# Kernel tuning notes

Measured on AMD Instinct MI355X. Metric: run time of the kernel, lower is better.

The kernel has to match this reference:

```python
import jax, jax.numpy as jnp
import numpy as np

N_NODES = 100000
N_EDGES = 1600000
N_FEATS = 128
N_CLASSES = 40
K_HOPS = 3


def setup_inputs() -> dict:
    key = jax.random.key(0)
    k1, k2, k3, k4 = jax.random.split(key, 4)
    x = jax.random.normal(k1, (N_NODES, N_FEATS), dtype=jnp.float32)
    edge_index = jax.random.randint(k2, (2, N_EDGES), 0, N_NODES, dtype=jnp.int64)
    edge_weight = jax.random.uniform(k3, (N_EDGES,), dtype=jnp.float32)
    # Linear layer of SGConv (bias=False): [num_feats, num_classes]
    W = jax.random.normal(k4, (N_FEATS, N_CLASSES), dtype=jnp.float32) / np.sqrt(N_FEATS)
    return {"x": x, "edge_index": edge_index, "edge_weight": edge_weight, "W": W}


def reference(x, edge_index, edge_weight, W):
    # SGConv forward: gcn_norm (symmetric, no self-loops), K hops of
    # edge-weighted gather/scatter aggregation, then linear (lin_first=False).
    row, col = edge_index[0], edge_index[1]
    # symmetric normalization: deg from target-node scatter of edge weights
    deg = jax.ops.segment_sum(edge_weight, col, num_segments=N_NODES)
    deg_inv_sqrt = jnp.where(deg > 0, jax.lax.rsqrt(jnp.maximum(deg, 1e-30)), 0.0)
    norm = deg_inv_sqrt[row] * edge_weight * deg_inv_sqrt[col]  # [E]
    h = x
    for _ in range(K_HOPS):
        msgs = h[row] * norm[:, None]                 # [E, F] gather + scale
        h = jax.ops.segment_sum(msgs, col, num_segments=N_NODES)  # [N, F] scatter-add
    return h @ W  # [N, num_classes]
```

## Files before the change

kernel.cpp:

```cpp
#include <hip/hip_runtime.h>
#include <hip/hip_fp16.h>

namespace {
constexpr int NN = 100000;
constexpr int NE = 1600000;
constexpr int NF = 128;
constexpr int NC = 40;
constexpr int HP = 64;
constexpr int NB = (NN + 255) / 256;
constexpr int EPB = 4096;
constexpr int EBK = (NE + EPB - 1) / EPB;
constexpr int CAP = 6144;
constexpr float FIX = 1048576.0f;
constexpr int NPB = 51;
constexpr int HB  = (NN + NPB - 1) / NPB;
constexpr int TS  = 2048;
}

struct alignas(16) H8 { __half2 a, b, c, d; };

__device__ inline __half2 f2h2(float x, float y) {
    return __halves2half2(__float2half_rn(x), __float2half_rn(y));
}

__global__ __launch_bounds__(256) void k_fused(const int* __restrict__ col,
                                               const int* __restrict__ row,
                                               const float* __restrict__ w,
                                               unsigned int* __restrict__ cursor,
                                               int2* __restrict__ bstage,
                                               const float* __restrict__ x,
                                               const float* __restrict__ W,
                                               __half* __restrict__ g0) {
    __shared__ char sb[20480];
    int t = threadIdx.x;
    if (blockIdx.x < (unsigned)EBK) {
        unsigned int* lhist = (unsigned int*)sb;
        unsigned int* lbase = lhist + NB;
        unsigned int* lrank = lbase + NB;
        for (int i = t; i < NB; i += 256) { lhist[i] = 0u; lrank[i] = 0u; }
        __syncthreads();
        int e0 = blockIdx.x * EPB;
        int e1 = min(e0 + EPB, NE);
        for (int e = e0 + t; e < e1; e += 256)
            atomicAdd(&lhist[col[e] >> 8], 1u);
        __syncthreads();
        for (int i = t; i < NB; i += 256) {
            unsigned c = lhist[i];
            lbase[i] = c ? atomicAdd(&cursor[i], c) : 0u;
        }
        __syncthreads();
        for (int e = e0 + t; e < e1; e += 256) {
            int c = col[e];
            int b = c >> 8;
            unsigned r = atomicAdd(&lrank[b], 1u);
            int2 v;
            v.x = (row[e] & 0x1FFFF) | ((c & 255) << 17);
            v.y = __float_as_int(w[e]);
            bstage[(size_t)b * CAP + lbase[b] + r] = v;
        }
    } else {
        float4* lW = (float4*)sb;
        {
            const float4* Wg = (const float4*)W;
#pragma unroll
            for (int i = 0; i < 5; ++i) lW[t + i * 256] = Wg[t + i * 256];
        }
        __syncthreads();
        int n = (blockIdx.x - EBK) * 256 + t;
        if (n >= NN) return;
        const float4* xr = (const float4*)(x + (size_t)n * NF);
        float acc[NC];
#pragma unroll
        for (int j = 0; j < NC; ++j) acc[j] = 0.f;
        for (int k4 = 0; k4 < NF / 4; ++k4) {
            float4 xv = xr[k4];
#pragma unroll
            for (int kk = 0; kk < 4; ++kk) {
                float xk = (kk == 0) ? xv.x : (kk == 1) ? xv.y : (kk == 2) ? xv.z : xv.w;
                int k = k4 * 4 + kk;
#pragma unroll
                for (int j4 = 0; j4 < 10; ++j4) {
                    float4 wv = lW[k * 10 + j4];
                    acc[j4 * 4 + 0] += xk * wv.x;
                    acc[j4 * 4 + 1] += xk * wv.y;
                    acc[j4 * 4 + 2] += xk * wv.z;
                    acc[j4 * 4 + 3] += xk * wv.w;
                }
            }
        }
        H8* o = (H8*)(g0 + (size_t)n * HP);
#pragma unroll
        for (int g = 0; g < 5; ++g) {
            H8 v;
            v.a = f2h2(acc[g * 8 + 0], acc[g * 8 + 1]);
            v.b = f2h2(acc[g * 8 + 2], acc[g * 8 + 3]);
            v.c = f2h2(acc[g * 8 + 4], acc[g * 8 + 5]);
            v.d = f2h2(acc[g * 8 + 6], acc[g * 8 + 7]);
            o[g] = v;
        }
    }
}

__global__ __launch_bounds__(512) void k_bscan(const unsigned int* __restrict__ cursor,
                                               int* __restrict__ bbase,
                                               int* __restrict__ offs) {
    __shared__ int s[512];
    int t = threadIdx.x;
    int v = (t < NB) ? (int)cursor[t] : 0;
    s[t] = v;
    __syncthreads();
    for (int off = 1; off < 512; off <<= 1) {
        int add = (t >= off) ? s[t - off] : 0;
        __syncthreads();
        s[t] += add;
        __syncthreads();
    }
    if (t < NB) bbase[t] = s[t] - v;
    if (t == NB) bbase[NB] = s[NB - 1];
    if (t == 0)  offs[NN] = NE;
}

__global__ __launch_bounds__(256) void k_sort(const int2* __restrict__ bstage,
                                              const int* __restrict__ bbase,
                                              int* __restrict__ offs,
                                              float* __restrict__ invdis,
                                              int2* __restrict__ pair,
                                              __half* __restrict__ g0) {
    __shared__ unsigned long long lpk[256];
    __shared__ int ls[256];
    __shared__ float ldis[256];
    __shared__ unsigned int lrank[256];
    int t = threadIdx.x;
    int b = blockIdx.x;
    int base = bbase[b];
    int cnt  = bbase[b + 1] - base;
    lpk[t] = 0ull;
    lrank[t] = 0u;
    __syncthreads();
    const int2* bs = bstage + (size_t)b * CAP;
    for (int j = t; j < cnt; j += 256) {
        int2 s = bs[j];
        int cl = (s.x >> 17) & 255;
        unsigned long long q =
            (unsigned long long)(unsigned)(__int_as_float(s.y) * FIX + 0.5f);
        atomicAdd(&lpk[cl], (1ull << 40) | q);
    }
    __syncthreads();
    int myc = (int)(lpk[t] >> 40);
    float deg = (float)(lpk[t] & ((1ull << 40) - 1)) * (1.0f / FIX);
    float dis = (deg > 0.f) ? rsqrtf(deg) : 0.f;
    ldis[t] = dis;
    ls[t] = myc;
    __syncthreads();
    for (int off = 1; off < 256; off <<= 1) {
        int add = (t >= off) ? ls[t - off] : 0;
        __syncthreads();
        ls[t] += add;
        __syncthreads();
    }
    int start = ls[t] - myc;
    int n = b * 256 + t;
    if (n < NN) {
        offs[n] = base + start;
        invdis[n] = sqrtf(fmaxf(deg, 0.f));
        *(float*)(g0 + (size_t)n * HP + 40) = dis;
    }
    ls[t] = start;
    __syncthreads();
    for (int j = t; j < cnt; j += 256) {
        int2 s = bs[j];
        int cl = (s.x >> 17) & 255;
        unsigned r = atomicAdd(&lrank[cl], 1u);
        float d = ldis[cl];
        int2 v;
        v.x = s.x & 0x1FFFF;
        v.y = __float_as_int(__int_as_float(s.y) * d * d);
        pair[base + ls[cl] + r] = v;
    }
}

template <bool FINAL, bool WD>
__global__ __launch_bounds__(256) void k_hop(const int* __restrict__ offs,
                                             const int2* __restrict__ pair,
                                             const __half* __restrict__ hin,
                                             __half* __restrict__ houth,
                                             float* __restrict__ houtf,
                                             const float* __restrict__ invdis) {
    __shared__ int2 tile[TS];
    __shared__ int erange[2];
    int t = threadIdx.x;
    int g = t / 5;
    int n = blockIdx.x * NPB + g;
    bool active = (t < NPB * 5) && (n < NN);
    int vo = (t - g * 5) * 8;
    int s0 = 0, s1 = 0;
    if (active) {
        s0 = offs[n];
        s1 = offs[n + 1];
    }
    if (t == 0) {
        int n0 = blockIdx.x * NPB;
        int nl = min(n0 + NPB, NN);
        erange[0] = offs[n0];
        erange[1] = offs[nl];
    }
    __syncthreads();
    int E0 = erange[0], E1 = erange[1];
    float acc[8];
#pragma unroll
    for (int j = 0; j < 8; ++j) acc[j] = 0.f;
    int i = s0;
#define ACC8(m, wgt) { float2 f_;                                        \
    f_ = __half22float2((m).a); acc[0] += f_.x * (wgt); acc[1] += f_.y * (wgt); \
    f_ = __half22float2((m).b); acc[2] += f_.x * (wgt); acc[3] += f_.y * (wgt); \
    f_ = __half22float2((m).c); acc[4] += f_.x * (wgt); acc[5] += f_.y * (wgt); \
    f_ = __half22float2((m).d); acc[6] += f_.x * (wgt); acc[7] += f_.y * (wgt); }
    for (int t0 = E0; t0 < E1; t0 += TS) {
        int lim = min(t0 + TS, E1);
        int cnt = lim - t0;
        for (int j = t; j < cnt; j += 256) tile[j] = pair[t0 + j];
        __syncthreads();
        if (active) {
            int hi = min(s1, lim);
            for (; i + 4 <= hi; i += 4) {
                int2 p0 = tile[i - t0];
                int2 p1 = tile[i + 1 - t0];
                int2 p2 = tile[i + 2 - t0];
                int2 p3 = tile[i + 3 - t0];
                const __half* r0 = hin + (size_t)p0.x * HP;
                const __half* r1 = hin + (size_t)p1.x * HP;
                const __half* r2 = hin + (size_t)p2.x * HP;
                const __half* r3 = hin + (size_t)p3.x * HP;
                H8 m0 = *(const H8*)(r0 + vo);
                H8 m1 = *(const H8*)(r1 + vo);
                H8 m2 = *(const H8*)(r2 + vo);
                H8 m3 = *(const H8*)(r3 + vo);
                float w0 = __int_as_float(p0.y);
                float w1 = __int_as_float(p1.y);
                float w2 = __int_as_float(p2.y);
                float w3 = __int_as_float(p3.y);
                if (WD) {
                    w0 *= *(const float*)(r0 + 40);
                    w1 *= *(const float*)(r1 + 40);
                    w2 *= *(const float*)(r2 + 40);
                    w3 *= *(const float*)(r3 + 40);
                }
                ACC8(m0, w0) ACC8(m1, w1) ACC8(m2, w2) ACC8(m3, w3)
            }
            for (; i < hi; ++i) {
                int2 p0 = tile[i - t0];
                const __half* r0 = hin + (size_t)p0.x * HP;
                H8 m0 = *(const H8*)(r0 + vo);
                float w0 = __int_as_float(p0.y);
                if (WD) w0 *= *(const float*)(r0 + 40);
                ACC8(m0, w0)
            }
        }
        __syncthreads();
    }
#undef ACC8
    if (active) {
        if (FINAL) {
            float sc = invdis[n];
            float* o = houtf + (size_t)n * NC + vo;
            float4 v0 = {acc[0] * sc, acc[1] * sc, acc[2] * sc, acc[3] * sc};
            float4 v1 = {acc[4] * sc, acc[5] * sc, acc[6] * sc, acc[7] * sc};
            *(float4*)(o) = v0;
            *(float4*)(o + 4) = v1;
        } else {
            H8 v;
            v.a = f2h2(acc[0], acc[1]);
            v.b = f2h2(acc[2], acc[3]);
            v.c = f2h2(acc[4], acc[5]);
            v.d = f2h2(acc[6], acc[7]);
            *(H8*)(houth + (size_t)n * HP + vo) = v;
        }
    }
}

extern "C" void kernel_launch(void* const* d_in, const int* in_sizes, int n_in,
                              void* d_out, int out_size, void* d_ws, size_t ws_size,
                              hipStream_t stream) {
    const float* x  = (const float*)d_in[0];
    const int*   ei = (const int*)d_in[1];
    const float* w  = (const float*)d_in[2];
    const float* W  = (const float*)d_in[3];
    const int* row = ei;
    const int* col = ei + NE;
    float* out = (float*)d_out;

    char* base = (char*)d_ws;
    int2* bstage = (int2*)base;
    __half* hb   = (__half*)base;
    char* p = base + (size_t)NB * CAP * 8;
    __half* ha = (__half*)p;        p += (size_t)NN * HP * 2;
    int2* pair = (int2*)p;          p += (size_t)NE * 8;
    int*  offs = (int*)p;           p += (size_t)(NN + 1) * 4;
    int*  bbase = (int*)p;          p += (size_t)(NB + 1) * 4;
    float* invdis = (float*)p;      p += (size_t)NN * 4;
    unsigned int* cursor = (unsigned int*)p;

    hipMemsetAsync(cursor, 0, (size_t)NB * 4, stream);
    k_fused<<<EBK + NB, 256, 0, stream>>>(col, row, w, cursor, bstage, x, W, ha);
    k_bscan<<<1, 512, 0, stream>>>(cursor, bbase, offs);
    k_sort<<<NB, 256, 0, stream>>>(bstage, bbase, offs, invdis, pair, ha);

    k_hop<false, true ><<<HB, 256, 0, stream>>>(offs, pair, ha, hb, nullptr, nullptr);
    k_hop<false, false><<<HB, 256, 0, stream>>>(offs, pair, hb, ha, nullptr, nullptr);
    k_hop<true,  false><<<HB, 256, 0, stream>>>(offs, pair, ha, nullptr, out, invdis);
}
```

Before: 267.3 us.

## Stage bucket records in LDS and reuse first-pass atomic ranks in sort

```diff
diff --git a/kernel.cpp b/kernel.cpp
--- a/kernel.cpp
+++ b/kernel.cpp
@@ -53,10 +53,11 @@
             int c = col[e];
             int b = c >> 8;
             unsigned r = atomicAdd(&lrank[b], 1u);
-            int2 v;
-            v.x = (row[e] & 0x1FFFF) | ((c & 255) << 17);
-            v.y = __float_as_int(w[e]);
-            bstage[(size_t)b * CAP + lbase[b] + r] = v;
+            unsigned long long u =
+                (unsigned long long)(unsigned)((row[e] & 0x1FFFF) | ((c & 255) << 17)) |
+                ((unsigned long long)(unsigned)__float_as_int(w[e]) << 32);
+            __builtin_nontemporal_store(
+                u, (unsigned long long*)(bstage + (size_t)b * CAP + lbase[b] + r));
         }
     } else {
         float4* lW = (float4*)sb;
@@ -120,62 +121,69 @@
     if (t == 0)  offs[NN] = NE;
 }
 
-__global__ __launch_bounds__(256) void k_sort(const int2* __restrict__ bstage,
+__global__ __launch_bounds__(512) void k_sort(const int2* __restrict__ bstage,
                                               const int* __restrict__ bbase,
                                               int* __restrict__ offs,
                                               float* __restrict__ invdis,
                                               int2* __restrict__ pair,
                                               __half* __restrict__ g0) {
+    __shared__ int2 rec[CAP];
+    __shared__ unsigned char rk8[CAP];
     __shared__ unsigned long long lpk[256];
     __shared__ int ls[256];
     __shared__ float ldis[256];
-    __shared__ unsigned int lrank[256];
     int t = threadIdx.x;
     int b = blockIdx.x;
     int base = bbase[b];
     int cnt  = bbase[b + 1] - base;
-    lpk[t] = 0ull;
-    lrank[t] = 0u;
-    __syncthreads();
-    const int2* bs = bstage + (size_t)b * CAP;
-    for (int j = t; j < cnt; j += 256) {
-        int2 s = bs[j];
+    if (t < 256) lpk[t] = 0ull;
+    __syncthreads();
+    const unsigned long long* bs64 = (const unsigned long long*)(bstage + (size_t)b * CAP);
+    for (int j = t; j < cnt; j += 512) {
+        unsigned long long u = __builtin_nontemporal_load(bs64 + j);
+        int2 s; s.x = (int)(unsigned)u; s.y = (int)(u >> 32);
+        rec[j] = s;
         int cl = (s.x >> 17) & 255;
         unsigned long long q =
             (unsigned long long)(unsigned)(__int_as_float(s.y) * FIX + 0.5f);
-        atomicAdd(&lpk[cl], (1ull << 40) | q);
-    }
-    __syncthreads();
-    int myc = (int)(lpk[t] >> 40);
-    float deg = (float)(lpk[t] & ((1ull << 40) - 1)) * (1.0f / FIX);
-    float dis = (deg > 0.f) ? rsqrtf(deg) : 0.f;
-    ldis[t] = dis;
-    ls[t] = myc;
+        unsigned long long old = atomicAdd(&lpk[cl], (1ull << 40) | q);
+        rk8[j] = (unsigned char)(old >> 40);
+    }
+    __syncthreads();
+    if (t < 256) {
+        int myc = (int)(lpk[t] >> 40);
+        float deg = (float)(lpk[t] & ((1ull << 40) - 1)) * (1.0f / FIX);
+        float dis = (deg > 0.f) ? rsqrtf(deg) : 0.f;
+        ldis[t] = dis;
+        ls[t] = myc;
+        int n = b * 256 + t;
+        if (n < NN) {
+            invdis[n] = sqrtf(fmaxf(deg, 0.f));
+            *(float*)(g0 + (size_t)n * HP + 40) = dis;
+        }
+    }
     __syncthreads();
     for (int off = 1; off < 256; off <<= 1) {
-        int add = (t >= off) ? ls[t - off] : 0;
-        __syncthreads();
-        ls[t] += add;
-        __syncthreads();
-    }
-    int start = ls[t] - myc;
-    int n = b * 256 + t;
-    if (n < NN) {
-        offs[n] = base + start;
-        invdis[n] = sqrtf(fmaxf(deg, 0.f));
-        *(float*)(g0 + (size_t)n * HP + 40) = dis;
-    }
-    ls[t] = start;
-    __syncthreads();
-    for (int j = t; j < cnt; j += 256) {
-        int2 s = bs[j];
+        int add = (t < 256 && t >= off) ? ls[t - off] : 0;
+        __syncthreads();
+        if (t < 256) ls[t] += add;
+        __syncthreads();
+    }
+    if (t < 256) {
+        int myc = (int)(lpk[t] >> 40);
+        ls[t] -= myc;
+        int n = b * 256 + t;
+        if (n < NN) offs[n] = base + ls[t];
+    }
+    __syncthreads();
+    for (int j = t; j < cnt; j += 512) {
+        int2 s = rec[j];
         int cl = (s.x >> 17) & 255;
-        unsigned r = atomicAdd(&lrank[cl], 1u);
         float d = ldis[cl];
         int2 v;
         v.x = s.x & 0x1FFFF;
         v.y = __float_as_int(__int_as_float(s.y) * d * d);
-        pair[base + ls[cl] + r] = v;
+        pair[base + ls[cl] + rk8[j]] = v;
     }
 }
 
@@ -303,7 +311,7 @@
     hipMemsetAsync(cursor, 0, (size_t)NB * 4, stream);
     k_fused<<<EBK + NB, 256, 0, stream>>>(col, row, w, cursor, bstage, x, W, ha);
     k_bscan<<<1, 512, 0, stream>>>(cursor, bbase, offs);
-    k_sort<<<NB, 256, 0, stream>>>(bstage, bbase, offs, invdis, pair, ha);
+    k_sort<<<NB, 512, 0, stream>>>(bstage, bbase, offs, invdis, pair, ha);
 
     k_hop<false, true ><<<HB, 256, 0, stream>>>(offs, pair, ha, hb, nullptr, nullptr);
     k_hop<false, false><<<HB, 256, 0, stream>>>(offs, pair, hb, ha, nullptr, nullptr);
```

Result: slower. 286.1 us (+7.0%).
